# Kernel tuning notes

Hardware: AMD Instinct MI355X
Metric: run time of the kernel (lower is better)

Reference implementation:

```python
import jax, jax.numpy as jnp
import numpy as np

B, T, I, H, HORIZON = 64, 512, 256, 1024, 24


def _lstm_layer(x, Wih, Whh, bih, bhh):
    """PyTorch-convention LSTM layer. x: [B,T,I_l] -> outputs [B,T,H].
    Gate order along 4H axis: i, f, g, o."""
    b = x.shape[0]
    h_dim = Whh.shape[1]
    # Precompute input contribution for all timesteps: [B,T,4H]
    xg = jnp.einsum('bti,gi->btg', x, Wih) + bih + bhh

    def step(carry, xg_t):
        h, c = carry
        gates = xg_t + h @ Whh.T  # [B,4H]
        i_g, f_g, g_g, o_g = jnp.split(gates, 4, axis=-1)
        c = jax.nn.sigmoid(f_g) * c + jax.nn.sigmoid(i_g) * jnp.tanh(g_g)
        h = jax.nn.sigmoid(o_g) * jnp.tanh(c)
        return (h, c), h

    h0 = jnp.zeros((b, h_dim), x.dtype)
    (_, _), hs = jax.lax.scan(step, (h0, h0), jnp.swapaxes(xg, 0, 1))
    return jnp.swapaxes(hs, 0, 1)  # [B,T,H]


def setup_inputs() -> dict:
    key = jax.random.key(0)
    ks = jax.random.split(key, 11)
    s_i = 1.0 / np.sqrt(H)  # PyTorch-style uniform-ish scale, use scaled normal
    return {
        'x': jax.random.normal(ks[0], (B, T, I), jnp.float32),
        'W_ih0': jax.random.normal(ks[1], (4 * H, I), jnp.float32) * s_i,
        'W_hh0': jax.random.normal(ks[2], (4 * H, H), jnp.float32) * s_i,
        'b_ih0': jax.random.normal(ks[3], (4 * H,), jnp.float32) * s_i,
        'b_hh0': jax.random.normal(ks[4], (4 * H,), jnp.float32) * s_i,
        'W_ih1': jax.random.normal(ks[5], (4 * H, H), jnp.float32) * s_i,
        'W_hh1': jax.random.normal(ks[6], (4 * H, H), jnp.float32) * s_i,
        'b_ih1': jax.random.normal(ks[7], (4 * H,), jnp.float32) * s_i,
        'b_hh1': jax.random.normal(ks[8], (4 * H,), jnp.float32) * s_i,
        'W_head': jax.random.normal(ks[9], (HORIZON, H), jnp.float32) * s_i,
        'b_head': jax.random.normal(ks[10], (HORIZON,), jnp.float32) * s_i,
    }


def reference(x, W_ih0, W_hh0, b_ih0, b_hh0, W_ih1, W_hh1, b_ih1, b_hh1, W_head, b_head):
    h1 = _lstm_layer(x, W_ih0, W_hh0, b_ih0, b_hh0)   # [B,T,H]
    h2 = _lstm_layer(h1, W_ih1, W_hh1, b_ih1, b_hh1)  # [B,T,H]
    last = h2[:, -1, :]                                # [B,H]
    return last @ W_head.T + b_head                    # [B,HORIZON]
```

## Files before the change

kernel.cpp:

```cpp
#include <hip/hip_runtime.h>


typedef _Float16 h8 __attribute__((ext_vector_type(8)));
typedef float    f4 __attribute__((ext_vector_type(4)));
typedef unsigned long long u64;

#define WS_W0P   0
#define WS_W1P   10485760
#define WS_H0Q   27262976
#define WS_H2Q   27787264
#define WS_SYNC  28049408
#define WS_XPK   28057600
#define WS_XPK_END 44834816ULL

static __device__ __forceinline__ float sigm(float v) { return 1.f / (1.f + __expf(-v)); }
static __device__ __forceinline__ float tanh_fast(float v) {
  const float e = __expf(2.f * v);
  return 1.f - 2.f / (e + 1.f);
}
static __device__ __forceinline__ h8 vload16(const _Float16* p) {
  return *(const volatile h8*)p;
}
static __device__ __forceinline__ void vstore16(_Float16* p, h8 v) {
  *(volatile h8*)p = v;
}

__global__ void prep_kernel(const float* __restrict__ x,
                            const float* __restrict__ Wih0, const float* __restrict__ Whh0,
                            const float* __restrict__ Wih1, const float* __restrict__ Whh1,
                            _Float16* __restrict__ W0p, _Float16* __restrict__ W1p,
                            _Float16* __restrict__ xpk,
                            unsigned* __restrict__ hz, unsigned* __restrict__ sync_ws)
{
  const long tid0 = (long)blockIdx.x * blockDim.x + threadIdx.x;
  const long np   = (long)gridDim.x * blockDim.x;

  for (long e = tid0; e < 5242880; e += np) {
    const int j = e & 7, quad = (e >> 3) & 3, l15 = (e >> 5) & 15, nt = (e >> 9) & 7;
    const int r = (int)(e >> 12);
    const int c = r % 40, cs = r / 40;
    const int col = nt * 16 + l15;
    const int row = (col >> 5) * 1024 + cs * 32 + (col & 31);
    const int k = c * 32 + quad * 8 + j;
    const float v = (k < 256) ? Wih0[(long)row * 256 + k] : Whh0[(long)row * 1024 + k - 256];
    W0p[e] = (_Float16)v;
  }
  for (long e = tid0; e < 8388608; e += np) {
    const int j = e & 7, quad = (e >> 3) & 3, l15 = (e >> 5) & 15, nt = (e >> 9) & 7;
    const int r = (int)(e >> 12);
    const int c = r & 63, cs = r >> 6;
    const int col = nt * 16 + l15;
    const int row = (col >> 5) * 1024 + cs * 32 + (col & 31);
    const int k = c * 32 + quad * 8 + j;
    const float v = (k < 1024) ? Wih1[(long)row * 1024 + k] : Whh1[(long)row * 1024 + k - 1024];
    W1p[e] = (_Float16)v;
  }
  if (xpk) {
    for (long e = tid0; e < 8388608; e += np) {
      const int k32 = e & 31, b16 = (e >> 5) & 15, bg = (e >> 9) & 3;
      const int c = (e >> 11) & 7;
      const int t = (int)(e >> 14);
      const int b = bg * 16 + b16, k = c * 32 + k32;
      xpk[e] = (_Float16)x[(long)b * 131072 + (long)t * 256 + k];
    }
  }
  for (long e = tid0; e < 196608; e += np) hz[e] = 0u;
  if (tid0 < 2048) sync_ws[tid0] = 0u;
}

template<bool XP>
__launch_bounds__(512, 1)
__global__ void lstm_kernel(const float* __restrict__ x, const _Float16* __restrict__ xpk,
                            const float* __restrict__ bih0, const float* __restrict__ bhh0,
                            const float* __restrict__ bih1, const float* __restrict__ bhh1,
                            const _Float16* __restrict__ W0p, const _Float16* __restrict__ W1p,
                            _Float16* __restrict__ h0q, _Float16* __restrict__ h2q,
                            unsigned* __restrict__ sy)
{
  extern __shared__ float gb[];
  __shared__ float cst[512];
  __shared__ float biasl[128];
  __shared__ _Float16 htmp[32 * 18];

  const int tid = threadIdx.x, wg = blockIdx.x;
  const int xcd = wg & 7, jdec = wg >> 3;
  const int lay = jdec & 1, jj = jdec >> 1;
  const int bg = jj & 3, csl = jj >> 2;
  const int cs = xcd * 4 + csl;
  const int lidx = bg * 32 + cs;
  const int g = lidx >> 3;
  const int lane = tid & 63, kg = tid >> 6;
  const int l15 = lane & 15, quad = lane >> 4;
  const int boff = l15 * 32 + quad * 8;
  const int aoff = bg * 512 + l15 * 32 + quad * 8;

  const _Float16* Wp = lay ? (W1p + (long)cs * 262144) : (W0p + (long)cs * 163840);

  if (tid < 128) {
    const int row = (tid >> 5) * 1024 + cs * 32 + (tid & 31);
    biasl[tid] = lay ? (bih1[row] + bhh1[row]) : (bih0[row] + bhh0[row]);
  }
  cst[tid] = 0.f;
  __syncthreads();

  unsigned* const own  = sy + lay * 1024;
  unsigned* const myF  = own + 512 + g * 16;
  unsigned* const otF  = sy + (1 - lay) * 1024 + 512 + g * 16;

  auto spin_ge = [&](const unsigned* p, int target) {
    while ((int)__hip_atomic_load(p, __ATOMIC_RELAXED, __HIP_MEMORY_SCOPE_AGENT) < target)
      __builtin_amdgcn_s_sleep(2);
  };
  auto arrive = [&](unsigned e) {
    const unsigned prev = __hip_atomic_fetch_add(own + g * 16, 1u,
                            __ATOMIC_RELAXED, __HIP_MEMORY_SCOPE_AGENT);
    if (prev == 8u * e - 1u) {
      const unsigned p2 = __hip_atomic_fetch_add(own + 384, 1u,
                            __ATOMIC_RELAXED, __HIP_MEMORY_SCOPE_AGENT);
      if (p2 == 16u * e - 1u) {
#pragma unroll
        for (int i = 0; i < 16; ++i)
          __hip_atomic_store(own + 512 + i * 16, e,
                             __ATOMIC_RELAXED, __HIP_MEMORY_SCOPE_AGENT);
      }
    }
  };

  auto dump = [&](const f4* acc) {
#pragma unroll
    for (int nt = 0; nt < 8; ++nt)
      *(f4*)&gb[(kg * 128 + nt * 16 + l15) * 20 + quad * 4] = acc[nt];
  };

  auto pointwise_publish = [&](_Float16* wr) {
    __syncthreads();
    {
      const int b16 = tid & 15, hh = tid >> 4;
      float gv[4];
#pragma unroll
      for (int gt = 0; gt < 4; ++gt) {
        float s = biasl[gt * 32 + hh];
#pragma unroll
        for (int k = 0; k < 8; ++k) s += gb[(k * 128 + gt * 32 + hh) * 20 + b16];
        gv[gt] = s;
      }
      const float si = sigm(gv[0]), sf = sigm(gv[1]);
      const float tg = tanh_fast(gv[2]), so = sigm(gv[3]);
      const float cn = sf * cst[tid] + si * tg;
      cst[tid] = cn;
      htmp[hh * 18 + b16] = (_Float16)(so * tanh_fast(cn));
    }
    __syncthreads();
    if (tid < 64) {
      const int b16 = tid & 15, q = tid >> 4;
      union { h8 v; _Float16 e[8]; } r;
#pragma unroll
      for (int i = 0; i < 8; ++i) r.e[i] = htmp[(q * 8 + i) * 18 + b16];
      vstore16(wr + (cs * 4 + bg) * 512 + b16 * 32 + q * 8, r.v);
    }
    __syncthreads();
  };

  if (lay == 0) {
    const int c0 = kg * 5;
    for (int n = 0; n < 512; ++n) {
      if (tid == 0) { spin_ge(myF, n); spin_ge(otF, n - 3); }
      __syncthreads();
      const _Float16* h0prev = h0q + ((n - 1) & 3) * 65536;
      const _Float16* xs = XP ? (xpk + (long)n * 16384) : nullptr;

      f4 acc[8] = {};
      h8 Ab[2]; h8 Bb[2][8];
      auto loadAB = [&](int i, int sl) {
        const int c = c0 + i;
        const _Float16* bp = Wp + (long)c * 4096 + boff;
#pragma unroll
        for (int nt = 0; nt < 8; ++nt) Bb[sl][nt] = *(const h8*)(bp + nt * 512);
        if (c < 8) {
          if (XP) Ab[sl] = *(const h8*)(xs + c * 2048 + aoff);
          else {
            const float* q = x + (long)(bg * 16 + l15) * 131072 + (long)n * 256 + c * 32 + quad * 8;
            const f4 v0 = *(const f4*)q;
            const f4 v1 = *(const f4*)(q + 4);
            h8 t;
            t[0]=(_Float16)v0[0]; t[1]=(_Float16)v0[1]; t[2]=(_Float16)v0[2]; t[3]=(_Float16)v0[3];
            t[4]=(_Float16)v1[0]; t[5]=(_Float16)v1[1]; t[6]=(_Float16)v1[2]; t[7]=(_Float16)v1[3];
            Ab[sl] = t;
          }
        } else {
          Ab[sl] = vload16(h0prev + (c - 8) * 2048 + aoff);
        }
      };
      loadAB(0, 0);
#pragma unroll
      for (int i = 0; i < 5; ++i) {
        if (i + 1 < 5) loadAB(i + 1, (i + 1) & 1);
        const h8 A = Ab[i & 1];
#pragma unroll
        for (int nt = 0; nt < 8; ++nt)
          acc[nt] = __builtin_amdgcn_mfma_f32_16x16x32_f16(A, Bb[i & 1][nt], acc[nt], 0, 0, 0);
      }
      dump(acc);
      pointwise_publish(h0q + (n & 3) * 65536);
      if (tid == 0) arrive((unsigned)n + 1u);
    }
  } else {
    const int c0 = kg * 4;
    for (int n = 0; n < 512; ++n) {
      if (tid == 0) spin_ge(otF, n + 1);
      __syncthreads();
      const _Float16* h0cur = h0q + (n & 3) * 65536;
      const _Float16* h2prev = h2q + ((n - 1) & 1) * 65536;

      f4 acc[8] = {};
      h8 Ab[2]; h8 Bb[2][8];
      auto loadAB = [&](const _Float16* hbase, int cw, int cloc, int sl) {
        const _Float16* bp = Wp + (long)cw * 4096 + boff;
#pragma unroll
        for (int nt = 0; nt < 8; ++nt) Bb[sl][nt] = *(const h8*)(bp + nt * 512);
        Ab[sl] = vload16(hbase + cloc * 2048 + aoff);
      };
      loadAB(h0cur, c0, c0, 0);
#pragma unroll
      for (int i = 0; i < 4; ++i) {
        if (i + 1 < 4) loadAB(h0cur, c0 + i + 1, c0 + i + 1, (i + 1) & 1);
        const h8 A = Ab[i & 1];
#pragma unroll
        for (int nt = 0; nt < 8; ++nt)
          acc[nt] = __builtin_amdgcn_mfma_f32_16x16x32_f16(A, Bb[i & 1][nt], acc[nt], 0, 0, 0);
      }
      if (tid == 0) spin_ge(myF, n);
      __syncthreads();
      loadAB(h2prev, 32 + c0, c0, 0);
#pragma unroll
      for (int i = 0; i < 4; ++i) {
        if (i + 1 < 4) loadAB(h2prev, 32 + c0 + i + 1, c0 + i + 1, (i + 1) & 1);
        const h8 A = Ab[i & 1];
#pragma unroll
        for (int nt = 0; nt < 8; ++nt)
          acc[nt] = __builtin_amdgcn_mfma_f32_16x16x32_f16(A, Bb[i & 1][nt], acc[nt], 0, 0, 0);
      }
      dump(acc);
      pointwise_publish(h2q + (n & 1) * 65536);
      if (tid == 0) arrive((unsigned)n + 1u);
    }
  }
}

__global__ void head_kernel(const _Float16* __restrict__ h2s, const float* __restrict__ Wh,
                            const float* __restrict__ bh, float* __restrict__ out)
{
  const int blk = blockIdx.x;
  const int b = blk / 24, j = blk % 24;
  const int lane = threadIdx.x;
  float sum = 0.f;
#pragma unroll
  for (int k0 = 0; k0 < 1024; k0 += 64) {
    const int hid = k0 + lane;
    const float hv = (float)h2s[((hid >> 5) * 4 + (b >> 4)) * 512 + (b & 15) * 32 + (hid & 31)];
    sum += hv * Wh[(long)j * 1024 + hid];
  }
#pragma unroll
  for (int off = 32; off > 0; off >>= 1)
    sum += __shfl_down(sum, off, 64);
  if (lane == 0) out[b * 24 + j] = sum + bh[j];
}

extern "C" void kernel_launch(void* const* d_in, const int* in_sizes, int n_in,
                              void* d_out, int out_size, void* d_ws, size_t ws_size,
                              hipStream_t stream)
{
  const float* x    = (const float*)d_in[0];
  const float* Wih0 = (const float*)d_in[1];
  const float* Whh0 = (const float*)d_in[2];
  const float* bih0 = (const float*)d_in[3];
  const float* bhh0 = (const float*)d_in[4];
  const float* Wih1 = (const float*)d_in[5];
  const float* Whh1 = (const float*)d_in[6];
  const float* bih1 = (const float*)d_in[7];
  const float* bhh1 = (const float*)d_in[8];
  const float* Whd  = (const float*)d_in[9];
  const float* bhd  = (const float*)d_in[10];

  char* ws = (char*)d_ws;
  _Float16* W0p     = (_Float16*)(ws + WS_W0P);
  _Float16* W1p     = (_Float16*)(ws + WS_W1P);
  _Float16* h0q     = (_Float16*)(ws + WS_H0Q);
  _Float16* h2q     = (_Float16*)(ws + WS_H2Q);
  unsigned* sync_ws = (unsigned*)(ws + WS_SYNC);
  float* out = (float*)d_out;

  const bool use_xpk = (ws_size >= WS_XPK_END);
  _Float16* xpk = use_xpk ? (_Float16*)(ws + WS_XPK) : nullptr;

  prep_kernel<<<dim3(2048), dim3(256), 0, stream>>>(
      x, Wih0, Whh0, Wih1, Whh1, W0p, W1p, xpk,
      (unsigned*)(ws + WS_H0Q), sync_ws);

  if (use_xpk)
    lstm_kernel<true><<<dim3(256), dim3(512), 81920, stream>>>(
        x, xpk, bih0, bhh0, bih1, bhh1, W0p, W1p, h0q, h2q, sync_ws);
  else
    lstm_kernel<false><<<dim3(256), dim3(512), 81920, stream>>>(
        x, nullptr, bih0, bhh0, bih1, bhh1, W0p, W1p, h0q, h2q, sync_ws);

  head_kernel<<<dim3(64 * 24), dim3(64), 0, stream>>>(
      h2q + 65536, Whd, bhd, out);
}
```

Baseline: 4.843 ms.

## Replace hierarchical grid barrier with per-block flags and prefetch before waiting

New measurement: 5.114 ms. 5.6% more time.

```diff
diff --git a/kernel.cpp b/kernel.cpp
--- a/kernel.cpp
+++ b/kernel.cpp
@@ -87,8 +87,6 @@
   const int lay = jdec & 1, jj = jdec >> 1;
   const int bg = jj & 3, csl = jj >> 2;
   const int cs = xcd * 4 + csl;
-  const int lidx = bg * 32 + cs;
-  const int g = lidx >> 3;
   const int lane = tid & 63, kg = tid >> 6;
   const int l15 = lane & 15, quad = lane >> 4;
   const int boff = l15 * 32 + quad * 8;
@@ -103,36 +101,23 @@
   cst[tid] = 0.f;
   __syncthreads();
 
-  unsigned* const own  = sy + lay * 1024;
-  unsigned* const myF  = own + 512 + g * 16;
-  unsigned* const otF  = sy + (1 - lay) * 1024 + 512 + g * 16;
-
-  auto spin_ge = [&](const unsigned* p, int target) {
-    while ((int)__hip_atomic_load(p, __ATOMIC_RELAXED, __HIP_MEMORY_SCOPE_AGENT) < target)
-      __builtin_amdgcn_s_sleep(2);
+  unsigned* const fL0  = sy + (bg * 32) * 8;
+  unsigned* const fL1  = sy + ((4 + bg) * 32) * 8;
+  unsigned* const fOwn = (lay ? fL1 : fL0) + cs * 8;
+
+  auto spin = [&](const unsigned* p, int tgt) {
+    if (tgt <= 0) return;
+    while ((int)__hip_atomic_load(p, __ATOMIC_RELAXED, __HIP_MEMORY_SCOPE_AGENT) < tgt)
+      __builtin_amdgcn_s_sleep(1);
   };
-  auto arrive = [&](unsigned e) {
-    const unsigned prev = __hip_atomic_fetch_add(own + g * 16, 1u,
-                            __ATOMIC_RELAXED, __HIP_MEMORY_SCOPE_AGENT);
-    if (prev == 8u * e - 1u) {
-      const unsigned p2 = __hip_atomic_fetch_add(own + 384, 1u,
-                            __ATOMIC_RELAXED, __HIP_MEMORY_SCOPE_AGENT);
-      if (p2 == 16u * e - 1u) {
-#pragma unroll
-        for (int i = 0; i < 16; ++i)
-          __hip_atomic_store(own + 512 + i * 16, e,
-                             __ATOMIC_RELAXED, __HIP_MEMORY_SCOPE_AGENT);
-      }
-    }
+
+  auto dump = [&](const f4* acc) {
+#pragma unroll
+    for (int nt = 0; nt < 8; ++nt)
+      *(f4*)&gb[(kg * 128 + nt * 16 + l15) * 24 + quad * 4] = acc[nt];
   };
 
-  auto dump = [&](const f4* acc) {
-#pragma unroll
-    for (int nt = 0; nt < 8; ++nt)
-      *(f4*)&gb[(kg * 128 + nt * 16 + l15) * 20 + quad * 4] = acc[nt];
-  };
-
-  auto pointwise_publish = [&](_Float16* wr) {
+  auto pointwise_publish = [&](_Float16* wr, int n) {
     __syncthreads();
     {
       const int b16 = tid & 15, hh = tid >> 4;
@@ -141,7 +126,7 @@
       for (int gt = 0; gt < 4; ++gt) {
         float s = biasl[gt * 32 + hh];
 #pragma unroll
-        for (int k = 0; k < 8; ++k) s += gb[(k * 128 + gt * 32 + hh) * 20 + b16];
+        for (int k = 0; k < 8; ++k) s += gb[(k * 128 + gt * 32 + hh) * 24 + b16];
         gv[gt] = s;
       }
       const float si = sigm(gv[0]), sf = sigm(gv[1]);
@@ -157,27 +142,29 @@
 #pragma unroll
       for (int i = 0; i < 8; ++i) r.e[i] = htmp[(q * 8 + i) * 18 + b16];
       vstore16(wr + (cs * 4 + bg) * 512 + b16 * 32 + q * 8, r.v);
-    }
-    __syncthreads();
+      asm volatile("s_waitcnt vmcnt(0)" ::: "memory");
+      if (tid == 0)
+        __hip_atomic_store(fOwn, (unsigned)(n + 1),
+                           __ATOMIC_RELAXED, __HIP_MEMORY_SCOPE_AGENT);
+    }
   };
 
   if (lay == 0) {
     const int c0 = kg * 5;
     for (int n = 0; n < 512; ++n) {
-      if (tid == 0) { spin_ge(myF, n); spin_ge(otF, n - 3); }
-      __syncthreads();
       const _Float16* h0prev = h0q + ((n - 1) & 3) * 65536;
       const _Float16* xs = XP ? (xpk + (long)n * 16384) : nullptr;
 
       f4 acc[8] = {};
-      h8 Ab[2]; h8 Bb[2][8];
-      auto loadAB = [&](int i, int sl) {
-        const int c = c0 + i;
+      h8 Ab[5]; h8 Bb[2][8];
+      auto loadB = [&](int c, int sl) {
         const _Float16* bp = Wp + (long)c * 4096 + boff;
 #pragma unroll
         for (int nt = 0; nt < 8; ++nt) Bb[sl][nt] = *(const h8*)(bp + nt * 512);
+      };
+      auto loadA = [&](int c, int idx) {
         if (c < 8) {
-          if (XP) Ab[sl] = *(const h8*)(xs + c * 2048 + aoff);
+          if (XP) Ab[idx] = *(const h8*)(xs + c * 2048 + aoff);
           else {
             const float* q = x + (long)(bg * 16 + l15) * 131072 + (long)n * 256 + c * 32 + quad * 8;
             const f4 v0 = *(const f4*)q;
@@ -185,64 +172,89 @@
             h8 t;
             t[0]=(_Float16)v0[0]; t[1]=(_Float16)v0[1]; t[2]=(_Float16)v0[2]; t[3]=(_Float16)v0[3];
             t[4]=(_Float16)v1[0]; t[5]=(_Float16)v1[1]; t[6]=(_Float16)v1[2]; t[7]=(_Float16)v1[3];
-            Ab[sl] = t;
+            Ab[idx] = t;
           }
         } else {
-          Ab[sl] = vload16(h0prev + (c - 8) * 2048 + aoff);
+          Ab[idx] = vload16(h0prev + (c - 8) * 2048 + aoff);
         }
       };
-      loadAB(0, 0);
+
+      loadB(c0, 0);
+#pragma unroll
+      for (int i = 0; i < 5; ++i)
+        if (c0 + i < 8) loadA(c0 + i, i);
+
+      if (kg == 1) {
+        if (lane < 32) spin(fL0 + lane * 8, n);
+        else           spin(fL1 + (lane - 32) * 8, n - 3);
+      }
+      __syncthreads();
+
+#pragma unroll
+      for (int i = 0; i < 5; ++i)
+        if (c0 + i >= 8) loadA(c0 + i, i);
+
 #pragma unroll
       for (int i = 0; i < 5; ++i) {
-        if (i + 1 < 5) loadAB(i + 1, (i + 1) & 1);
-        const h8 A = Ab[i & 1];
+        if (i + 1 < 5) loadB(c0 + i + 1, (i + 1) & 1);
+        const h8 A = Ab[i];
 #pragma unroll
         for (int nt = 0; nt < 8; ++nt)
           acc[nt] = __builtin_amdgcn_mfma_f32_16x16x32_f16(A, Bb[i & 1][nt], acc[nt], 0, 0, 0);
       }
       dump(acc);
-      pointwise_publish(h0q + (n & 3) * 65536);
-      if (tid == 0) arrive((unsigned)n + 1u);
+      pointwise_publish(h0q + (n & 3) * 65536, n);
     }
   } else {
     const int c0 = kg * 4;
     for (int n = 0; n < 512; ++n) {
-      if (tid == 0) spin_ge(otF, n + 1);
+      const _Float16* h0cur  = h0q + (n & 3) * 65536;
+      const _Float16* h2prev = h2q + ((n - 1) & 1) * 65536;
+
+      f4 acc[8] = {};
+      h8 Ab[4]; h8 Bb[2][8];
+      auto loadB = [&](int c, int sl) {
+        const _Float16* bp = Wp + (long)c * 4096 + boff;
+#pragma unroll
+        for (int nt = 0; nt < 8; ++nt) Bb[sl][nt] = *(const h8*)(bp + nt * 512);
+      };
+      auto loadA = [&](const _Float16* hb, int cloc, int idx) {
+        Ab[idx] = vload16(hb + cloc * 2048 + aoff);
+      };
+
+      loadB(32 + c0, 0);
+      if (kg == 1) {
+        if (lane < 32) spin(fL1 + lane * 8, n);
+      }
       __syncthreads();
-      const _Float16* h0cur = h0q + (n & 3) * 65536;
-      const _Float16* h2prev = h2q + ((n - 1) & 1) * 65536;
-
-      f4 acc[8] = {};
-      h8 Ab[2]; h8 Bb[2][8];
-      auto loadAB = [&](const _Float16* hbase, int cw, int cloc, int sl) {
-        const _Float16* bp = Wp + (long)cw * 4096 + boff;
-#pragma unroll
-        for (int nt = 0; nt < 8; ++nt) Bb[sl][nt] = *(const h8*)(bp + nt * 512);
-        Ab[sl] = vload16(hbase + cloc * 2048 + aoff);
-      };
-      loadAB(h0cur, c0, c0, 0);
+#pragma unroll
+      for (int i = 0; i < 4; ++i) loadA(h2prev, c0 + i, i);
 #pragma unroll
       for (int i = 0; i < 4; ++i) {
-        if (i + 1 < 4) loadAB(h0cur, c0 + i + 1, c0 + i + 1, (i + 1) & 1);
-        const h8 A = Ab[i & 1];
+        if (i + 1 < 4) loadB(32 + c0 + i + 1, (i + 1) & 1);
+        const h8 A = Ab[i];
 #pragma unroll
         for (int nt = 0; nt < 8; ++nt)
           acc[nt] = __builtin_amdgcn_mfma_f32_16x16x32_f16(A, Bb[i & 1][nt], acc[nt], 0, 0, 0);
       }
-      if (tid == 0) spin_ge(myF, n);
+
+      loadB(c0, 0);
+      if (kg == 1) {
+        if (lane < 32) spin(fL0 + lane * 8, n + 1);
+      }
       __syncthreads();
-      loadAB(h2prev, 32 + c0, c0, 0);
+#pragma unroll
+      for (int i = 0; i < 4; ++i) loadA(h0cur, c0 + i, i);
 #pragma unroll
       for (int i = 0; i < 4; ++i) {
-        if (i + 1 < 4) loadAB(h2prev, 32 + c0 + i + 1, c0 + i + 1, (i + 1) & 1);
-        const h8 A = Ab[i & 1];
+        if (i + 1 < 4) loadB(c0 + i + 1, (i + 1) & 1);
+        const h8 A = Ab[i];
 #pragma unroll
         for (int nt = 0; nt < 8; ++nt)
           acc[nt] = __builtin_amdgcn_mfma_f32_16x16x32_f16(A, Bb[i & 1][nt], acc[nt], 0, 0, 0);
       }
       dump(acc);
-      pointwise_publish(h2q + (n & 1) * 65536);
-      if (tid == 0) arrive((unsigned)n + 1u);
+      pointwise_publish(h2q + (n & 1) * 65536, n);
     }
   }
 }
@@ -298,10 +310,10 @@
       (unsigned*)(ws + WS_H0Q), sync_ws);
 
   if (use_xpk)
-    lstm_kernel<true><<<dim3(256), dim3(512), 81920, stream>>>(
+    lstm_kernel<true><<<dim3(256), dim3(512), 98304, stream>>>(
         x, xpk, bih0, bhh0, bih1, bhh1, W0p, W1p, h0q, h2q, sync_ws);
   else
-    lstm_kernel<false><<<dim3(256), dim3(512), 81920, stream>>>(
+    lstm_kernel<false><<<dim3(256), dim3(512), 98304, stream>>>(
         x, nullptr, bih0, bhh0, bih1, bhh1, W0p, W1p, h0q, h2q, sync_ws);
 
   head_kernel<<<dim3(64 * 24), dim3(64), 0, stream>>>(
```
